# Performance work log

Hardware: AMD Instinct MI355X
Metric: run time of the kernel (lower is better)

## Reference

```python
import jax, jax.numpy as jnp
import numpy as np

D_MODEL = 1024
NUM_HEADS = 16
D_HEAD = D_MODEL // NUM_HEADS
BATCH = 4
SEQ = 2048
NEG_INF = -1e30


def setup_inputs() -> dict:
    key = jax.random.key(0)
    k_x, k_q, k_k, k_v, k_o = jax.random.split(key, 5)
    scale = 1.0 / np.sqrt(D_MODEL)
    x = jax.random.normal(k_x, (BATCH, SEQ, D_MODEL), dtype=jnp.float32)
    Qw = jax.random.normal(k_q, (D_MODEL, D_MODEL), dtype=jnp.float32) * scale
    Kw = jax.random.normal(k_k, (D_MODEL, D_MODEL), dtype=jnp.float32) * scale
    Vw = jax.random.normal(k_v, (D_MODEL, D_MODEL), dtype=jnp.float32) * scale
    Ow = jax.random.normal(k_o, (D_MODEL, D_MODEL), dtype=jnp.float32) * scale
    padding_mask = jnp.zeros((BATCH, SEQ), dtype=bool)  # True = masked position
    return {"x": x, "Qw": Qw, "Kw": Kw, "Vw": Vw, "Ow": Ow, "padding_mask": padding_mask}


def reference(x, Qw, Kw, Vw, Ow, padding_mask):
    B, S, D = x.shape
    H, dh = NUM_HEADS, D_HEAD
    # torch Linear (no bias): y = x @ W.T
    q = jnp.einsum("bsd,ed->bse", x, Qw).reshape(B, S, H, dh)
    k = jnp.einsum("bsd,ed->bse", x, Kw).reshape(B, S, H, dh)
    v = jnp.einsum("bsd,ed->bse", x, Vw).reshape(B, S, H, dh)
    # scores: [B, H, Sq, Sk]
    score = jnp.einsum("bqhd,bkhd->bhqk", q, k) / jnp.sqrt(jnp.float32(dh))
    # causal mask (masked=True)
    causal = jnp.tril(jnp.ones((S, S), dtype=bool))  # True = keep
    score = jnp.where(causal[None, None, :, :], score, NEG_INF)
    # padding mask: True = masked key position
    score = jnp.where(padding_mask[:, None, None, :], NEG_INF, score)
    attn = jax.nn.softmax(score, axis=-1)  # dropout=0.0 (eval mode)
    ctx = jnp.einsum("bhqk,bkhd->bqhd", attn, v).reshape(B, S, D)
    out = jnp.einsum("bsd,ed->bse", ctx, Ow)
    return out
```

## Files before the change

### kernel.cpp

```cpp
#include <hip/hip_runtime.h>
#include <hip/hip_bf16.h>

typedef __attribute__((ext_vector_type(8))) short short8;
typedef __attribute__((ext_vector_type(4))) float f32x4;

#define MFMA_BF16_16x16x32(a,b,c) __builtin_amdgcn_mfma_f32_16x16x32_bf16((a),(b),(c),0,0,0)

constexpr int B_  = 4;
constexpr int S_  = 2048;
constexpr int H_  = 16;
constexpr int DH_ = 64;
constexpr int D_  = 1024;
constexpr int M_  = B_ * S_;

__device__ __forceinline__ unsigned short f2bf(float f) {
  union { float f; unsigned u; } v; v.f = f;
  unsigned u = v.u;
  u += 0x7fffu + ((u >> 16) & 1u);
  return (unsigned short)(u >> 16);
}

__device__ __forceinline__ short8 cvt8(f32x4 a, f32x4 b) {
  union { __hip_bfloat162 h[4]; short8 s; } u;
  u.h[0] = __float22bfloat162_rn(make_float2(a[0], a[1]));
  u.h[1] = __float22bfloat162_rn(make_float2(a[2], a[3]));
  u.h[2] = __float22bfloat162_rn(make_float2(b[0], b[1]));
  u.h[3] = __float22bfloat162_rn(make_float2(b[2], b[3]));
  return u.s;
}

__device__ __forceinline__ unsigned pk2(float a, float b) {
  union { __hip_bfloat162 h; unsigned u; } z;
  z.h = __float22bfloat162_rn(make_float2(a, b));
  return z.u;
}

__global__ __launch_bounds__(256)
void cvt_x(const float* __restrict__ x, unsigned short* __restrict__ xb) {
  const size_t i = ((size_t)blockIdx.x * 256 + threadIdx.x) * 8;
  *(short8*)(xb + i) = cvt8(*(const f32x4*)(x + i), *(const f32x4*)(x + i + 4));
}

__global__ __launch_bounds__(256)
void cvt_w(const float* __restrict__ s0, const float* __restrict__ s1,
           const float* __restrict__ s2,
           unsigned short* __restrict__ d0, unsigned short* __restrict__ d1,
           unsigned short* __restrict__ d2) {
  const int a = blockIdx.x >> 9;
  const float* s = (a == 0) ? s0 : (a == 1) ? s1 : s2;
  unsigned short* d = (a == 0) ? d0 : (a == 1) ? d1 : d2;
  const size_t i = ((size_t)(blockIdx.x & 511) * 256 + threadIdx.x) * 8;
  *(short8*)(d + i) = cvt8(*(const f32x4*)(s + i), *(const f32x4*)(s + i + 4));
}

__device__ __forceinline__ void stage16(const unsigned short* __restrict__ g,
                                        short* lds_wave_base, int lane) {
#if __has_builtin(__builtin_amdgcn_global_load_lds)
  __builtin_amdgcn_global_load_lds(
      (const __attribute__((address_space(1))) unsigned int*)g,
      (__attribute__((address_space(3))) unsigned int*)lds_wave_base, 16, 0, 0);
#else
  *(short8*)(lds_wave_base + lane * 8) = *(const short8*)g;
#endif
}

__global__ __launch_bounds__(256)
void gemm_bb(const unsigned short* __restrict__ xb,
             const unsigned short* __restrict__ Qwb,
             const unsigned short* __restrict__ Kwb,
             const unsigned short* __restrict__ Vwb,
             unsigned short* __restrict__ Qo, unsigned short* __restrict__ Ko,
             unsigned short* __restrict__ VTo, int haveQ) {
  __shared__ __align__(16) short As[128 * 32];
  __shared__ __align__(16) short Bs[128 * 32];

  const int nb  = blockIdx.x;
  const int sel = haveQ ? (nb >> 3) : 1 + (nb >> 3);
  const int n0  = (nb & 7) * 128;
  const unsigned short* Wb = (sel == 0) ? Qwb : (sel == 1) ? Kwb : Vwb;
  unsigned short* out      = (sel == 0) ? Qo  : (sel == 1) ? Ko  : VTo;
  const float scale = (sel == 0) ? 0.125f : 1.0f;
  const int epi = (sel == 2) ? 2 : 1;

  const int tid  = threadIdx.x;
  const int lane = tid & 63;
  const int w    = tid >> 6;
  const int quad = lane >> 4;
  const int l16  = lane & 15;
  const int wm   = (w >> 1) * 64;
  const int wn   = (w & 1) * 64;
  const int m0   = blockIdx.y * 128;

  const int srow = tid >> 2;
  const int scol = (tid & 3) * 8;

  f32x4 acc[4][4];
  #pragma unroll
  for (int i = 0; i < 4; ++i)
    #pragma unroll
    for (int j = 0; j < 4; ++j)
      acc[i][j] = (f32x4){0.f, 0.f, 0.f, 0.f};

  for (int k0 = 0; k0 < D_; k0 += 32) {
    __syncthreads();
    #pragma unroll
    for (int j = 0; j < 2; ++j) {
      const int row = j * 64 + srow;
      stage16(xb + (size_t)(m0 + row) * D_ + k0 + scol, As + j * 2048 + w * 512, lane);
      stage16(Wb + (size_t)(n0 + row) * D_ + k0 + scol, Bs + j * 2048 + w * 512, lane);
    }
    __syncthreads();

    short8 af[4], bf[4];
    #pragma unroll
    for (int i = 0; i < 4; ++i)
      af[i] = *(const short8*)(&As[(wm + i * 16 + l16) * 32 + quad * 8]);
    #pragma unroll
    for (int j = 0; j < 4; ++j)
      bf[j] = *(const short8*)(&Bs[(wn + j * 16 + l16) * 32 + quad * 8]);
    #pragma unroll
    for (int i = 0; i < 4; ++i)
      #pragma unroll
      for (int j = 0; j < 4; ++j)
        acc[i][j] = MFMA_BF16_16x16x32(af[i], bf[j], acc[i][j]);
  }

  #pragma unroll
  for (int i = 0; i < 4; ++i)
    #pragma unroll
    for (int j = 0; j < 4; ++j)
      #pragma unroll
      for (int r = 0; r < 4; ++r) {
        int m = m0 + wm + i * 16 + quad * 4 + r;
        int n = n0 + wn + j * 16 + l16;
        unsigned short bv = f2bf(acc[i][j][r] * scale);
        int b = m >> 11, s = m & (S_ - 1);
        int h = n >> 6,  d = n & (DH_ - 1);
        if (epi == 1)
          out[((size_t)(b * H_ + h) * S_ + s) * DH_ + d] = bv;
        else
          out[((size_t)(b * H_ + h) * DH_ + d) * S_ + s] = bv;
      }
}

__global__ __launch_bounds__(256)
void gemm_out_bb(const unsigned short* __restrict__ A,
                 const unsigned short* __restrict__ Wb,
                 float* __restrict__ out) {
  __shared__ __align__(16) short As[128 * 32];
  __shared__ __align__(16) short Bs[128 * 32];

  const int tid  = threadIdx.x;
  const int lane = tid & 63;
  const int w    = tid >> 6;
  const int quad = lane >> 4;
  const int l16  = lane & 15;
  const int wm   = (w >> 1) * 64;
  const int wn   = (w & 1) * 64;
  const int m0   = blockIdx.y * 128;
  const int n0   = blockIdx.x * 128;

  const int srow = tid >> 2;
  const int scol = (tid & 3) * 8;

  f32x4 acc[4][4];
  #pragma unroll
  for (int i = 0; i < 4; ++i)
    #pragma unroll
    for (int j = 0; j < 4; ++j)
      acc[i][j] = (f32x4){0.f, 0.f, 0.f, 0.f};

  for (int k0 = 0; k0 < D_; k0 += 32) {
    __syncthreads();
    #pragma unroll
    for (int j = 0; j < 2; ++j) {
      const int row = j * 64 + srow;
      stage16(A  + (size_t)(m0 + row) * D_ + k0 + scol, As + j * 2048 + w * 512, lane);
      stage16(Wb + (size_t)(n0 + row) * D_ + k0 + scol, Bs + j * 2048 + w * 512, lane);
    }
    __syncthreads();

    short8 af[4], bf[4];
    #pragma unroll
    for (int i = 0; i < 4; ++i)
      af[i] = *(const short8*)(&As[(wm + i * 16 + l16) * 32 + quad * 8]);
    #pragma unroll
    for (int j = 0; j < 4; ++j)
      bf[j] = *(const short8*)(&Bs[(wn + j * 16 + l16) * 32 + quad * 8]);
    #pragma unroll
    for (int i = 0; i < 4; ++i)
      #pragma unroll
      for (int j = 0; j < 4; ++j)
        acc[i][j] = MFMA_BF16_16x16x32(af[i], bf[j], acc[i][j]);
  }

  #pragma unroll
  for (int i = 0; i < 4; ++i)
    #pragma unroll
    for (int j = 0; j < 4; ++j)
      #pragma unroll
      for (int r = 0; r < 4; ++r) {
        int m = m0 + wm + i * 16 + quad * 4 + r;
        int n = n0 + wn + j * 16 + l16;
        out[(size_t)m * D_ + n] = acc[i][j][r];
      }
}

__global__ __launch_bounds__(256)
void gemm_q_f32w(const unsigned short* __restrict__ xb,
                 const float* __restrict__ Qw,
                 unsigned short* __restrict__ Qo) {
  constexpr int LDK = 40;
  __shared__ __align__(16) short As[128 * LDK];
  __shared__ __align__(16) short Bs[128 * LDK];

  const int tid  = threadIdx.x;
  const int lane = tid & 63;
  const int w    = tid >> 6;
  const int quad = lane >> 4;
  const int l16  = lane & 15;
  const int wm   = (w >> 1) * 64;
  const int wn   = (w & 1) * 64;
  const int m0   = blockIdx.y * 128;
  const int n0   = blockIdx.x * 128;

  f32x4 acc[4][4];
  #pragma unroll
  for (int i = 0; i < 4; ++i)
    #pragma unroll
    for (int j = 0; j < 4; ++j)
      acc[i][j] = (f32x4){0.f, 0.f, 0.f, 0.f};

  for (int k0 = 0; k0 < D_; k0 += 32) {
    __syncthreads();
    #pragma unroll
    for (int i = 0; i < 2; ++i) {
      int flat = i * 256 + tid;
      int row  = flat >> 2;
      int col  = (flat & 3) * 8;
      *(short8*)(&As[row * LDK + col]) =
          *(const short8*)(xb + (size_t)(m0 + row) * D_ + k0 + col);
      const float* Wp = Qw + (size_t)(n0 + row) * D_ + k0 + col;
      *(short8*)(&Bs[row * LDK + col]) = cvt8(*(const f32x4*)Wp, *(const f32x4*)(Wp + 4));
    }
    __syncthreads();

    short8 af[4], bf[4];
    #pragma unroll
    for (int i = 0; i < 4; ++i)
      af[i] = *(const short8*)(&As[(wm + i * 16 + l16) * LDK + quad * 8]);
    #pragma unroll
    for (int j = 0; j < 4; ++j)
      bf[j] = *(const short8*)(&Bs[(wn + j * 16 + l16) * LDK + quad * 8]);
    #pragma unroll
    for (int i = 0; i < 4; ++i)
      #pragma unroll
      for (int j = 0; j < 4; ++j)
        acc[i][j] = MFMA_BF16_16x16x32(af[i], bf[j], acc[i][j]);
  }

  #pragma unroll
  for (int i = 0; i < 4; ++i)
    #pragma unroll
    for (int j = 0; j < 4; ++j)
      #pragma unroll
      for (int r = 0; r < 4; ++r) {
        int m = m0 + wm + i * 16 + quad * 4 + r;
        int n = n0 + wn + j * 16 + l16;
        unsigned short bv = f2bf(acc[i][j][r] * 0.125f);
        int b = m >> 11, s = m & (S_ - 1);
        int h = n >> 6,  d = n & (DH_ - 1);
        Qo[((size_t)(b * H_ + h) * S_ + s) * DH_ + d] = bv;
      }
}

constexpr int LDP_ = 72;

__device__ __forceinline__ void attn_range(
    const unsigned short* __restrict__ Kh,
    const unsigned short* __restrict__ Vh,
    const unsigned char* __restrict__ pmb,
    short* __restrict__ Pw,
    const short8 qf[2][2], f32x4 acc[2][4], f32x4 lacc[2],
    int qw, int kt0, int kt1, int quad, int l16) {
  const short8 ones = {0x3F80, 0x3F80, 0x3F80, 0x3F80,
                       0x3F80, 0x3F80, 0x3F80, 0x3F80};
  for (int kt = kt0; kt < kt1; ++kt) {
    const int k0 = kt * 64;

    short8 kb[8];
    #pragma unroll
    for (int t = 0; t < 4; ++t) {
      const unsigned short* kp = Kh + (size_t)(k0 + t * 16 + l16) * DH_ + quad * 8;
      kb[t * 2]     = *(const short8*)(kp);
      kb[t * 2 + 1] = *(const short8*)(kp + 32);
    }
    unsigned pm4[4];
    #pragma unroll
    for (int t = 0; t < 4; ++t)
      pm4[t] = *(const unsigned*)(pmb + k0 + t * 16 + quad * 4);

    f32x4 sc[2][4];
    __builtin_amdgcn_s_setprio(1);
    #pragma unroll
    for (int t = 0; t < 4; ++t) {
      #pragma unroll
      for (int i = 0; i < 2; ++i) {
        f32x4 z = (f32x4){0.f, 0.f, 0.f, 0.f};
        z = MFMA_BF16_16x16x32(kb[t * 2], qf[i][0], z);
        sc[i][t] = MFMA_BF16_16x16x32(kb[t * 2 + 1], qf[i][1], z);
      }
    }
    __builtin_amdgcn_s_setprio(0);

    short8 vb[8];
    #pragma unroll
    for (int t = 0; t < 4; ++t)
      vb[t] = *(const short8*)(Vh + (size_t)(t * 16 + l16) * S_ + k0 + quad * 8);

    #pragma unroll
    for (int i = 0; i < 2; ++i)
      #pragma unroll
      for (int t = 0; t < 4; ++t)
        #pragma unroll
        for (int r = 0; r < 4; ++r) {
          float e = __expf(sc[i][t][r]);
          sc[i][t][r] = ((pm4[t] >> (8 * r)) & 0xffu) ? 0.f : e;
        }
    if (k0 + 63 > qw) {
      #pragma unroll
      for (int t = 0; t < 4; ++t)
        #pragma unroll
        for (int r = 0; r < 4; ++r) {
          int key = k0 + t * 16 + quad * 4 + r;
          #pragma unroll
          for (int i = 0; i < 2; ++i) {
            int qrow = qw + i * 16 + l16;
            if (key > qrow) sc[i][t][r] = 0.f;
          }
        }
    }

    #pragma unroll
    for (int i = 0; i < 2; ++i)
      #pragma unroll
      for (int t = 0; t < 4; ++t) {
        unsigned lo = pk2(sc[i][t][0], sc[i][t][1]);
        unsigned hi = pk2(sc[i][t][2], sc[i][t][3]);
        *(uint2*)(&Pw[(i * 16 + l16) * LDP_ + t * 16 + quad * 4]) = make_uint2(lo, hi);
      }

    #pragma unroll
    for (int t = 0; t < 4; ++t)
      vb[4 + t] = *(const short8*)(Vh + (size_t)(t * 16 + l16) * S_ + k0 + 32 + quad * 8);

    __builtin_amdgcn_s_setprio(1);
    #pragma unroll
    for (int ks = 0; ks < 2; ++ks) {
      short8 pa0 = *(const short8*)(&Pw[l16 * LDP_ + ks * 32 + quad * 8]);
      short8 pa1 = *(const short8*)(&Pw[(16 + l16) * LDP_ + ks * 32 + quad * 8]);
      #pragma unroll
      for (int t = 0; t < 4; ++t) {
        acc[0][t] = MFMA_BF16_16x16x32(pa0, vb[ks * 4 + t], acc[0][t]);
        acc[1][t] = MFMA_BF16_16x16x32(pa1, vb[ks * 4 + t], acc[1][t]);
      }
      lacc[0] = MFMA_BF16_16x16x32(pa0, ones, lacc[0]);
      lacc[1] = MFMA_BF16_16x16x32(pa1, ones, lacc[1]);
    }
    __builtin_amdgcn_s_setprio(0);
  }
}

__global__ __launch_bounds__(128)
void attn(const unsigned short* __restrict__ Q,
          const unsigned short* __restrict__ K,
          const unsigned short* __restrict__ VT,
          const unsigned char* __restrict__ pmask,
          unsigned short* __restrict__ CTX) {
  __shared__ __align__(16) short Ps[2 * 32 * LDP_];
  __shared__ float Rbuf[64 * 40];

  const int tid  = threadIdx.x;
  const int lane = tid & 63;
  const int w    = tid >> 6;
  const int quad = lane >> 4;
  const int l16  = lane & 15;

  const int L    = blockIdx.x;
  const int xcd  = L & 7;
  const int slot = L >> 3;
  const int bh   = xcd + 8 * (slot & 7);
  const int p    = slot >> 3;
  const int b    = bh >> 4;
  const int h    = bh & 15;

  const int qtA = p, qtB = 63 - p;
  const int ntA = (qtA >> 1) + 1;
  const int ntB = (qtB >> 1) + 1;
  const int splitB = 17 - ntA;

  const unsigned short* Qh = Q  + ((size_t)b * H_ + h) * S_ * DH_;
  const unsigned short* Kh = K  + ((size_t)b * H_ + h) * S_ * DH_;
  const unsigned short* Vh = VT + ((size_t)b * H_ + h) * DH_ * S_;
  const unsigned char* pmb = pmask + (size_t)b * S_;
  unsigned short* CTXb = CTX + (size_t)b * S_ * D_;
  short* Pw = &Ps[w * 32 * LDP_];

  f32x4 acc[2][4];
  f32x4 lacc[2];
  short8 qf[2][2];

  if (w == 0) {
    {
      const int qw = qtA * 32;
      #pragma unroll
      for (int i = 0; i < 2; ++i)
        #pragma unroll
        for (int c = 0; c < 2; ++c)
          qf[i][c] = *(const short8*)(Qh + (size_t)(qw + i * 16 + l16) * DH_ + c * 32 + quad * 8);
      #pragma unroll
      for (int i = 0; i < 2; ++i) {
        #pragma unroll
        for (int t = 0; t < 4; ++t) acc[i][t] = (f32x4){0.f, 0.f, 0.f, 0.f};
        lacc[i] = (f32x4){0.f, 0.f, 0.f, 0.f};
      }
      attn_range(Kh, Vh, pmb, Pw, qf, acc, lacc, qw, 0, ntA, quad, l16);
      #pragma unroll
      for (int i = 0; i < 2; ++i)
        #pragma unroll
        for (int r = 0; r < 4; ++r) {
          int qrow = qw + i * 16 + quad * 4 + r;
          float inv = 1.0f / lacc[i][r];
          #pragma unroll
          for (int t = 0; t < 4; ++t)
            CTXb[(size_t)qrow * D_ + h * DH_ + t * 16 + l16] = f2bf(acc[i][t][r] * inv);
        }
    }
    {
      const int qw = qtB * 32;
      #pragma unroll
      for (int i = 0; i < 2; ++i)
        #pragma unroll
        for (int c = 0; c < 2; ++c)
          qf[i][c] = *(const short8*)(Qh + (size_t)(qw + i * 16 + l16) * DH_ + c * 32 + quad * 8);
      #pragma unroll
      for (int i = 0; i < 2; ++i) {
        #pragma unroll
        for (int t = 0; t < 4; ++t) acc[i][t] = (f32x4){0.f, 0.f, 0.f, 0.f};
        lacc[i] = (f32x4){0.f, 0.f, 0.f, 0.f};
      }
      attn_range(Kh, Vh, pmb, Pw, qf, acc, lacc, qw, 0, splitB, quad, l16);
      __syncthreads();
      #pragma unroll
      for (int i = 0; i < 2; ++i) {
        #pragma unroll
        for (int t = 0; t < 4; ++t)
          #pragma unroll
          for (int r = 0; r < 4; ++r)
            acc[i][t][r] += Rbuf[lane * 40 + i * 16 + t * 4 + r];
        #pragma unroll
        for (int r = 0; r < 4; ++r)
          lacc[i][r] += Rbuf[lane * 40 + 32 + i * 4 + r];
      }
      #pragma unroll
      for (int i = 0; i < 2; ++i)
        #pragma unroll
        for (int r = 0; r < 4; ++r) {
          int qrow = qw + i * 16 + quad * 4 + r;
          float inv = 1.0f / lacc[i][r];
          #pragma unroll
          for (int t = 0; t < 4; ++t)
            CTXb[(size_t)qrow * D_ + h * DH_ + t * 16 + l16] = f2bf(acc[i][t][r] * inv);
        }
    }
  } else {
    const int qw = qtB * 32;
    #pragma unroll
    for (int i = 0; i < 2; ++i)
      #pragma unroll
      for (int c = 0; c < 2; ++c)
        qf[i][c] = *(const short8*)(Qh + (size_t)(qw + i * 16 + l16) * DH_ + c * 32 + quad * 8);
    #pragma unroll
    for (int i = 0; i < 2; ++i) {
      #pragma unroll
      for (int t = 0; t < 4; ++t) acc[i][t] = (f32x4){0.f, 0.f, 0.f, 0.f};
      lacc[i] = (f32x4){0.f, 0.f, 0.f, 0.f};
    }
    attn_range(Kh, Vh, pmb, Pw, qf, acc, lacc, qw, splitB, ntB, quad, l16);
    #pragma unroll
    for (int i = 0; i < 2; ++i) {
      #pragma unroll
      for (int t = 0; t < 4; ++t)
        #pragma unroll
        for (int r = 0; r < 4; ++r)
          Rbuf[lane * 40 + i * 16 + t * 4 + r] = acc[i][t][r];
      #pragma unroll
      for (int r = 0; r < 4; ++r)
        Rbuf[lane * 40 + 32 + i * 4 + r] = lacc[i][r];
    }
    __syncthreads();
  }
}

extern "C" void kernel_launch(void* const* d_in, const int* in_sizes, int n_in,
                              void* d_out, int out_size, void* d_ws, size_t ws_size,
                              hipStream_t stream) {
  const float* x  = (const float*)d_in[0];
  const float* Qw = (const float*)d_in[1];
  const float* Kw = (const float*)d_in[2];
  const float* Vw = (const float*)d_in[3];
  const float* Ow = (const float*)d_in[4];
  const unsigned char* pm = (const unsigned char*)d_in[5];

  const size_t NE = (size_t)M_ * D_;
  const size_t DD = (size_t)D_ * D_;
  unsigned short* Qall  = (unsigned short*)d_out;
  unsigned short* CTXa  = (unsigned short*)d_out + NE;
  unsigned short* ws16  = (unsigned short*)d_ws;
  unsigned short* Kall  = ws16;
  unsigned short* VTall = ws16 + NE;
  unsigned short* Owb   = VTall;

  const bool tail = ws_size >= (2 * NE + 3 * DD) * sizeof(unsigned short);

  cvt_x<<<dim3((unsigned)(NE / 2048)), 256, 0, stream>>>(x, CTXa);

  if (tail) {
    unsigned short* Qwb = ws16 + 2 * NE;
    unsigned short* Kwb = Qwb + DD;
    unsigned short* Vwb = Kwb + DD;
    cvt_w<<<dim3(3 * 512), 256, 0, stream>>>(Qw, Kw, Vw, Qwb, Kwb, Vwb);
    gemm_bb<<<dim3(24, M_ / 128), 256, 0, stream>>>(CTXa, Qwb, Kwb, Vwb,
                                                    Qall, Kall, VTall, 1);
  } else {
    unsigned short* Kwb = Qall;
    unsigned short* Vwb = Qall + DD;
    cvt_w<<<dim3(2 * 512), 256, 0, stream>>>(Kw, Vw, Vw, Kwb, Vwb, Vwb);
    gemm_bb<<<dim3(16, M_ / 128), 256, 0, stream>>>(CTXa, nullptr, Kwb, Vwb,
                                                    Qall, Kall, VTall, 0);
    gemm_q_f32w<<<dim3(8, M_ / 128), 256, 0, stream>>>(CTXa, Qw, Qall);
  }

  attn<<<dim3(2048), 128, 0, stream>>>(Qall, Kall, VTall, pm, CTXa);

  cvt_w<<<dim3(512), 256, 0, stream>>>(Ow, Ow, Ow, Owb, Owb, Owb);

  hipMemcpyAsync(d_ws, (const void*)CTXa, NE * sizeof(unsigned short),
                 hipMemcpyDeviceToDevice, stream);

  gemm_out_bb<<<dim3(D_ / 128, M_ / 128), 256, 0, stream>>>(ws16, Owb,
                                                            (float*)d_out);
}
```

Baseline: 349.7 us.

## Prefetch next K tile, swizzle P scratch, merge x/weight conversion into one launch

The attention inner loop now loads the next iteration's K fragments before the PV MFMAs, so K global loads overlap compute. The P staging buffer drops its padded stride in favour of an XOR swizzle, which is meant to avoid LDS bank conflicts while using less LDS. The x, Kw and Vw fp32-to-bf16 conversions are merged into one kernel launch. The host also always takes the path that reads the fp32 Q weight directly in gemm_q_f32w instead of converting it, which may slow the Q projection when the larger workspace was available.

```diff
diff --git a/kernel.cpp b/kernel.cpp
--- a/kernel.cpp
+++ b/kernel.cpp
@@ -36,21 +36,23 @@
 }
 
 __global__ __launch_bounds__(256)
-void cvt_x(const float* __restrict__ x, unsigned short* __restrict__ xb) {
+void cvt_pre(const float* __restrict__ x, unsigned short* __restrict__ xb,
+             const float* __restrict__ Kw, const float* __restrict__ Vw,
+             unsigned short* __restrict__ Kwb, unsigned short* __restrict__ Vwb) {
+  const int bb = blockIdx.x;
+  const float* s;
+  unsigned short* d;
+  size_t i;
+  if (bb < 4096)      { s = x;  d = xb;  i = ((size_t)bb * 256 + threadIdx.x) * 8; }
+  else if (bb < 4608) { s = Kw; d = Kwb; i = ((size_t)(bb - 4096) * 256 + threadIdx.x) * 8; }
+  else                { s = Vw; d = Vwb; i = ((size_t)(bb - 4608) * 256 + threadIdx.x) * 8; }
+  *(short8*)(d + i) = cvt8(*(const f32x4*)(s + i), *(const f32x4*)(s + i + 4));
+}
+
+__global__ __launch_bounds__(256)
+void cvt_w(const float* __restrict__ s0, unsigned short* __restrict__ d0) {
   const size_t i = ((size_t)blockIdx.x * 256 + threadIdx.x) * 8;
-  *(short8*)(xb + i) = cvt8(*(const f32x4*)(x + i), *(const f32x4*)(x + i + 4));
-}
-
-__global__ __launch_bounds__(256)
-void cvt_w(const float* __restrict__ s0, const float* __restrict__ s1,
-           const float* __restrict__ s2,
-           unsigned short* __restrict__ d0, unsigned short* __restrict__ d1,
-           unsigned short* __restrict__ d2) {
-  const int a = blockIdx.x >> 9;
-  const float* s = (a == 0) ? s0 : (a == 1) ? s1 : s2;
-  unsigned short* d = (a == 0) ? d0 : (a == 1) ? d1 : d2;
-  const size_t i = ((size_t)(blockIdx.x & 511) * 256 + threadIdx.x) * 8;
-  *(short8*)(d + i) = cvt8(*(const f32x4*)(s + i), *(const f32x4*)(s + i + 4));
+  *(short8*)(d0 + i) = cvt8(*(const f32x4*)(s0 + i), *(const f32x4*)(s0 + i + 4));
 }
 
 __device__ __forceinline__ void stage16(const unsigned short* __restrict__ g,
@@ -274,7 +276,7 @@
       }
 }
 
-constexpr int LDP_ = 72;
+constexpr int LDP_ = 64;
 
 __device__ __forceinline__ void attn_range(
     const unsigned short* __restrict__ Kh,
@@ -285,16 +287,23 @@
     int qw, int kt0, int kt1, int quad, int l16) {
   const short8 ones = {0x3F80, 0x3F80, 0x3F80, 0x3F80,
                        0x3F80, 0x3F80, 0x3F80, 0x3F80};
-  for (int kt = kt0; kt < kt1; ++kt) {
-    const int k0 = kt * 64;
-
-    short8 kb[8];
+  if (kt0 >= kt1) return;
+  const int key = (l16 & 7) << 4;
+
+  short8 kb[8];
+  {
+    const int k0 = kt0 * 64;
     #pragma unroll
     for (int t = 0; t < 4; ++t) {
       const unsigned short* kp = Kh + (size_t)(k0 + t * 16 + l16) * DH_ + quad * 8;
       kb[t * 2]     = *(const short8*)(kp);
       kb[t * 2 + 1] = *(const short8*)(kp + 32);
     }
+  }
+
+  for (int kt = kt0; kt < kt1; ++kt) {
+    const int k0 = kt * 64;
+
     unsigned pm4[4];
     #pragma unroll
     for (int t = 0; t < 4; ++t)
@@ -332,11 +341,11 @@
       for (int t = 0; t < 4; ++t)
         #pragma unroll
         for (int r = 0; r < 4; ++r) {
-          int key = k0 + t * 16 + quad * 4 + r;
+          int kk = k0 + t * 16 + quad * 4 + r;
           #pragma unroll
           for (int i = 0; i < 2; ++i) {
             int qrow = qw + i * 16 + l16;
-            if (key > qrow) sc[i][t][r] = 0.f;
+            if (kk > qrow) sc[i][t][r] = 0.f;
           }
         }
     }
@@ -347,8 +356,20 @@
       for (int t = 0; t < 4; ++t) {
         unsigned lo = pk2(sc[i][t][0], sc[i][t][1]);
         unsigned hi = pk2(sc[i][t][2], sc[i][t][3]);
-        *(uint2*)(&Pw[(i * 16 + l16) * LDP_ + t * 16 + quad * 4]) = make_uint2(lo, hi);
-      }
+        int boff = (i * 16 + l16) * 128 + ((t * 32 + quad * 8) ^ key);
+        *(uint2*)((char*)Pw + boff) = make_uint2(lo, hi);
+      }
+
+    asm volatile("" ::: "memory");
+    {
+      const int kn = (kt + 1 < kt1) ? (kt + 1) * 64 : k0;
+      #pragma unroll
+      for (int t = 0; t < 4; ++t) {
+        const unsigned short* kp = Kh + (size_t)(kn + t * 16 + l16) * DH_ + quad * 8;
+        kb[t * 2]     = *(const short8*)(kp);
+        kb[t * 2 + 1] = *(const short8*)(kp + 32);
+      }
+    }
 
     #pragma unroll
     for (int t = 0; t < 4; ++t)
@@ -357,8 +378,10 @@
     __builtin_amdgcn_s_setprio(1);
     #pragma unroll
     for (int ks = 0; ks < 2; ++ks) {
-      short8 pa0 = *(const short8*)(&Pw[l16 * LDP_ + ks * 32 + quad * 8]);
-      short8 pa1 = *(const short8*)(&Pw[(16 + l16) * LDP_ + ks * 32 + quad * 8]);
+      short8 pa0 = *(const short8*)((const char*)Pw +
+                    (l16 * 128 + ((ks * 64 + quad * 16) ^ key)));
+      short8 pa1 = *(const short8*)((const char*)Pw +
+                    ((16 + l16) * 128 + ((ks * 64 + quad * 16) ^ key)));
       #pragma unroll
       for (int t = 0; t < 4; ++t) {
         acc[0][t] = MFMA_BF16_16x16x32(pa0, vb[ks * 4 + t], acc[0][t]);
@@ -521,29 +544,18 @@
   unsigned short* VTall = ws16 + NE;
   unsigned short* Owb   = VTall;
 
-  const bool tail = ws_size >= (2 * NE + 3 * DD) * sizeof(unsigned short);
-
-  cvt_x<<<dim3((unsigned)(NE / 2048)), 256, 0, stream>>>(x, CTXa);
-
-  if (tail) {
-    unsigned short* Qwb = ws16 + 2 * NE;
-    unsigned short* Kwb = Qwb + DD;
-    unsigned short* Vwb = Kwb + DD;
-    cvt_w<<<dim3(3 * 512), 256, 0, stream>>>(Qw, Kw, Vw, Qwb, Kwb, Vwb);
-    gemm_bb<<<dim3(24, M_ / 128), 256, 0, stream>>>(CTXa, Qwb, Kwb, Vwb,
-                                                    Qall, Kall, VTall, 1);
-  } else {
-    unsigned short* Kwb = Qall;
-    unsigned short* Vwb = Qall + DD;
-    cvt_w<<<dim3(2 * 512), 256, 0, stream>>>(Kw, Vw, Vw, Kwb, Vwb, Vwb);
-    gemm_bb<<<dim3(16, M_ / 128), 256, 0, stream>>>(CTXa, nullptr, Kwb, Vwb,
-                                                    Qall, Kall, VTall, 0);
-    gemm_q_f32w<<<dim3(8, M_ / 128), 256, 0, stream>>>(CTXa, Qw, Qall);
-  }
+  unsigned short* Kwb = Qall;
+  unsigned short* Vwb = Qall + DD;
+
+  cvt_pre<<<dim3(4096 + 1024), 256, 0, stream>>>(x, CTXa, Kw, Vw, Kwb, Vwb);
+
+  gemm_bb<<<dim3(16, M_ / 128), 256, 0, stream>>>(CTXa, nullptr, Kwb, Vwb,
+                                                  Qall, Kall, VTall, 0);
+  gemm_q_f32w<<<dim3(8, M_ / 128), 256, 0, stream>>>(CTXa, Qw, Qall);
 
   attn<<<dim3(2048), 128, 0, stream>>>(Qall, Kall, VTall, pm, CTXa);
 
-  cvt_w<<<dim3(512), 256, 0, stream>>>(Ow, Ow, Ow, Owb, Owb, Owb);
+  cvt_w<<<dim3(512), 256, 0, stream>>>(Ow, Owb);
 
   hipMemcpyAsync(d_ws, (const void*)CTXa, NE * sizeof(unsigned short),
                  hipMemcpyDeviceToDevice, stream);
```

Result: slower. 378.6 us (+8.3%).
